# Performance work log

Hardware: AMD Instinct MI355X
Metric: run time of the kernel (lower is better)

Reference implementation:

```python
import jax, jax.numpy as jnp
import numpy as np

B, T, C, H = 2, 2048, 1024, 16
HD = C // H          # head_dim = 64
RD = HD // 2         # rotary half-dim = 32


def _rope_tables(T, rd, base=10000.0):
    inv_freq = 1.0 / (base ** (np.arange(rd, dtype=np.float32) / rd))
    t = np.arange(T, dtype=np.float32)
    ang = np.outer(t, inv_freq)  # [T, rd]
    cos = np.cos(ang)[None, :, None, :]  # [1,T,1,rd]
    sin = np.sin(ang)[None, :, None, :]
    return jnp.asarray(cos), jnp.asarray(sin)


def setup_inputs() -> dict:
    key = jax.random.key(0)
    k1, k2, k3 = jax.random.split(key, 3)
    cos, sin = _rope_tables(T, RD)
    return {
        "x": jax.random.normal(k1, (B, T, C), dtype=jnp.float32),
        "cos": cos,
        "sin": sin,
        "W_qkv": jax.random.normal(k2, (C, C), dtype=jnp.float32) / np.sqrt(C),
        "W_proj": jax.random.normal(k3, (C, C), dtype=jnp.float32) / np.sqrt(C),
        "window_left": 512,
    }


def _apply_rotary(x, cos, sin):
    # x: [B,T,H,HD]
    x1, x2 = x[..., :RD], x[..., RD:]
    y1 = x1 * cos + x2 * sin
    y2 = -x1 * sin + x2 * cos
    return jnp.concatenate([y1, y2], axis=-1)


def _rms_norm(x):
    eps = jnp.finfo(x.dtype).eps
    ms = jnp.mean(jnp.square(x), axis=-1, keepdims=True)
    return x * jax.lax.rsqrt(ms + eps)


def reference(x, cos, sin, W_qkv, W_proj, window_left):
    Bx, Tx, Cx = x.shape
    scale = HD ** -0.5
    # tied QKV projection (single matmul)
    w = jnp.einsum("btc,cd->btd", x, W_qkv).reshape(Bx, Tx, H, HD)
    w = _apply_rotary(w, cos, sin)
    w = _rms_norm(w)                      # [B,T,H,HD]
    wq = jnp.transpose(w, (0, 2, 1, 3))    # [B,H,T,HD]
    dots = jnp.einsum("bhqd,bhkd->bhqk", wq, wq) * scale  # [B,H,T,T]
    # causal + sliding-window mask: allow 0 <= (q - k) <= window_left
    i = jnp.arange(Tx)[:, None]
    j = jnp.arange(Tx)[None, :]
    dist = i - j
    allowed = (dist >= 0) & ((window_left <= 0) | (dist <= window_left))
    dots = jnp.where(allowed, dots, -jnp.inf)
    attn = jax.nn.softmax(dots, axis=-1)
    out = jnp.einsum("bhqk,bhkd->bhqd", attn, wq)
    out = jnp.transpose(out, (0, 2, 1, 3)).reshape(Bx, Tx, Cx)
    return jnp.einsum("btc,cd->btd", out, W_proj)
```

## Files before the change

kernel.cpp:

```cpp
#include <hip/hip_runtime.h>
#include <hip/hip_bf16.h>

typedef __bf16 bf16_t;
typedef __bf16 bf16x4 __attribute__((ext_vector_type(4)));
typedef __bf16 bf16x8 __attribute__((ext_vector_type(8)));
typedef float f32x4 __attribute__((ext_vector_type(4)));

#define B_ 2
#define T_ 2048
#define C_ 1024
#define H_ 16
#define HD_ 64
#define RD_ 32
#define M_ (B_ * T_)

__global__ __launch_bounds__(256) void k_prep(const float* __restrict__ x,
                                              bf16_t* __restrict__ xb,
                                              const float* __restrict__ Wq,
                                              bf16_t* __restrict__ wqt,
                                              const float* __restrict__ Wp,
                                              bf16_t* __restrict__ wpt) {
    const int bid = blockIdx.x;
    if (bid < 4096) {
        int i = bid * 256 + threadIdx.x;
        float4 v = reinterpret_cast<const float4*>(x)[i];
        bf16x4 o;
        o[0] = (bf16_t)v.x; o[1] = (bf16_t)v.y; o[2] = (bf16_t)v.z; o[3] = (bf16_t)v.w;
        reinterpret_cast<bf16x4*>(xb)[i] = o;
    } else {
        __shared__ float tile[32][33];
        int b2 = bid - 4096;
        const float* W = (b2 < 1024) ? Wq : Wp;
        bf16_t* Wt = (b2 < 1024) ? wqt : wpt;
        b2 &= 1023;
        const int n0 = (b2 & 31) * 32, k0 = (b2 >> 5) * 32;
        const int tx = threadIdx.x & 31, ty = threadIdx.x >> 5;
        for (int i = ty; i < 32; i += 8)
            tile[i][tx] = W[(size_t)(k0 + i) * C_ + n0 + tx];
        __syncthreads();
        for (int i = ty; i < 32; i += 8)
            Wt[(size_t)(n0 + i) * C_ + k0 + tx] = (bf16_t)tile[tx][i];
    }
}

template <bool FUSED>
__global__ __launch_bounds__(256) void k_gemm(const bf16_t* __restrict__ A,
                                              const bf16_t* __restrict__ Bt,
                                              float* __restrict__ C,
                                              const float* __restrict__ ct,
                                              const float* __restrict__ st,
                                              bf16_t* __restrict__ qp,
                                              bf16_t* __restrict__ vp,
                                              int M, int N, int K) {
    constexpr int SMEM_BYTES = FUSED ? 52224 : 49152;
    __shared__ __align__(16) char smem[SMEM_BYTES];
    bf16_t* As = (bf16_t*)smem;
    bf16_t* Bs = (bf16_t*)(smem + 32768);
    const int tid = threadIdx.x;
    const int lane = tid & 63, w = tid >> 6;
    const int wr = w >> 1, wc = w & 1;
    const int g = lane >> 4, li = lane & 15;
    const int bid = blockIdx.x;
    const int work = (bid & 7) * 64 + (bid >> 3);
    const int bx = work & 15;
    const int by = work >> 4;
    const size_t rowA0 = (size_t)by * 128;
    const size_t colB0 = (size_t)bx * 64;
    const bf16_t* Ab = A + rowA0 * K;
    const bf16_t* Bb = Bt + colB0 * K;
    f32x4 acc[4][2] = {};

    const int lr = lane >> 3;
    const int swc = ((lane & 7) ^ lr) * 8;

    auto stage = [&](int buf, int k0) {
        bf16_t* Ad = As + buf * 8192 + (w * 8) * 64;
        bf16_t* Bd = Bs + buf * 4096 + (w * 8) * 64;
#pragma unroll
        for (int a = 0; a < 4; ++a) {
            const bf16_t* src = Ab + (size_t)(a * 32 + w * 8 + lr) * K + k0 + swc;
            __builtin_amdgcn_global_load_lds(
                (const __attribute__((address_space(1))) void*)src,
                (__attribute__((address_space(3))) void*)(Ad + a * 32 * 64), 16, 0, 0);
        }
#pragma unroll
        for (int bq = 0; bq < 2; ++bq) {
            const bf16_t* src = Bb + (size_t)(bq * 32 + w * 8 + lr) * K + k0 + swc;
            __builtin_amdgcn_global_load_lds(
                (const __attribute__((address_space(1))) void*)src,
                (__attribute__((address_space(3))) void*)(Bd + bq * 32 * 64), 16, 0, 0);
        }
    };

    stage(0, 0);
    __syncthreads();
    int cur = 0;
    const int NT = K >> 6;
    for (int kt = 0; kt < NT; ++kt) {
        if (kt < NT - 1) stage(cur ^ 1, (kt + 1) << 6);
        bf16x8 af[4][2], bfr[2][2];
#pragma unroll
        for (int i = 0; i < 4; ++i) {
            const int row = wr * 64 + i * 16 + li;
#pragma unroll
            for (int kk = 0; kk < 2; ++kk)
                af[i][kk] = *(const bf16x8*)(As + cur * 8192 + row * 64 +
                                             (((kk * 4 + g) ^ (li & 7)) * 8));
        }
#pragma unroll
        for (int j = 0; j < 2; ++j) {
            const int row = wc * 32 + j * 16 + li;
#pragma unroll
            for (int kk = 0; kk < 2; ++kk)
                bfr[j][kk] = *(const bf16x8*)(Bs + cur * 4096 + row * 64 +
                                              (((kk * 4 + g) ^ (li & 7)) * 8));
        }
#pragma unroll
        for (int i = 0; i < 4; ++i)
#pragma unroll
            for (int j = 0; j < 2; ++j)
#pragma unroll
                for (int kk = 0; kk < 2; ++kk)
                    acc[i][j] = __builtin_amdgcn_mfma_f32_16x16x32_bf16(
                        af[i][kk], bfr[j][kk], acc[i][j], 0, 0, 0);
        __syncthreads();
        cur ^= 1;
    }

    if constexpr (!FUSED) {
#pragma unroll
        for (int i = 0; i < 4; ++i)
#pragma unroll
            for (int j = 0; j < 2; ++j)
#pragma unroll
                for (int r = 0; r < 4; ++r) {
                    size_t row = rowA0 + wr * 64 + i * 16 + g * 4 + r;
                    size_t col = colB0 + wc * 32 + j * 16 + li;
                    C[row * N + col] = acc[i][j][r];
                }
    } else {
        float* ot = (float*)smem;
        bf16_t* qs = (bf16_t*)(smem + 34816);
#pragma unroll
        for (int i = 0; i < 4; ++i)
#pragma unroll
            for (int j = 0; j < 2; ++j)
#pragma unroll
                for (int r = 0; r < 4; ++r)
                    ot[(wr * 64 + i * 16 + g * 4 + r) * 68 + wc * 32 + j * 16 + li] =
                        acc[i][j][r];
        __syncthreads();
        const int bb = (int)(rowA0 >> 11);
        {
            const int row = tid >> 1, half = tid & 1;
            const int t = ((int)rowA0 + row) & 2047;
            const float* own = ot + row * 68 + half * 32;
            const float* par = ot + row * 68 + (half ^ 1) * 32;
            const float* cp = ct + (size_t)t * RD_;
            const float* sp = st + (size_t)t * RD_;
            float y[32];
            float sq = 0.f;
#pragma unroll
            for (int c4 = 0; c4 < 8; ++c4) {
                float4 xo = ((const float4*)own)[c4];
                float4 xp = ((const float4*)par)[c4];
                float4 cc = ((const float4*)cp)[c4];
                float4 ss = ((const float4*)sp)[c4];
                float* yy = y + c4 * 4;
                if (half == 0) {
                    yy[0] = xo.x * cc.x + xp.x * ss.x;
                    yy[1] = xo.y * cc.y + xp.y * ss.y;
                    yy[2] = xo.z * cc.z + xp.z * ss.z;
                    yy[3] = xo.w * cc.w + xp.w * ss.w;
                } else {
                    yy[0] = xo.x * cc.x - xp.x * ss.x;
                    yy[1] = xo.y * cc.y - xp.y * ss.y;
                    yy[2] = xo.z * cc.z - xp.z * ss.z;
                    yy[3] = xo.w * cc.w - xp.w * ss.w;
                }
                sq += yy[0] * yy[0] + yy[1] * yy[1] + yy[2] * yy[2] + yy[3] * yy[3];
            }
            sq += __shfl_xor(sq, 1);
            const float rn = rsqrtf(sq * (1.0f / 64.0f) + 1.1920929e-7f);
            bf16_t yb[32];
#pragma unroll
            for (int e = 0; e < 32; ++e) yb[e] = (bf16_t)(y[e] * rn);
            bf16_t* qpb = qp + ((size_t)(bb * H_ + bx) * 128 + (t >> 4)) * 1024;
#pragma unroll
            for (int c8 = 0; c8 < 4; ++c8) {
                const int chunk = (half * 4 + c8) * 16 + (t & 15);
                *(bf16x8*)(qpb + chunk * 8) = *(const bf16x8*)(yb + c8 * 8);
            }
#pragma unroll
            for (int e = 0; e < 32; ++e)
                qs[(half * 32 + e) * 136 + row] = yb[e];
        }
        __syncthreads();
        {
            const int d = tid >> 2, jc4 = tid & 3;
            const int tt0 = (int)((rowA0 & 2047) >> 6);
            bf16_t* vpb = vp + ((size_t)(bb * H_ + bx) * 32) * 4096;
#pragma unroll
            for (int c = 0; c < 4; ++c) {
                const int jc = jc4 * 4 + c;
                bf16x8 v8 = *(const bf16x8*)(qs + d * 136 + jc * 8);
                bf16_t* dst = vpb + (size_t)(tt0 + (jc >> 3)) * 4096 +
                              ((d >> 4) * 8 + (jc & 7)) * 128 + (d & 15) * 8;
                *(bf16x8*)dst = v8;
            }
        }
    }
}

__global__ __launch_bounds__(256, 4) void k_attn(const bf16_t* __restrict__ qp,
                                                 const bf16_t* __restrict__ vp,
                                                 bf16_t* __restrict__ aout,
                                                 const int* __restrict__ wlp) {
    __shared__ bf16_t pb[4][16][40];
    const int tid = threadIdx.x;
    const int lane = tid & 63, w = tid >> 6;
    const int g = lane >> 4, li = lane & 15;
    const int bid = blockIdx.x;
    const int work = (bid & 7) * 128 + (bid >> 3);
    const int tb = work & 31;
    const int h = (work >> 5) & 15;
    const int b = work >> 9;
    const int Q0 = tb * 64;
    const bf16_t* bq = qp + (size_t)(b * H_ + h) * 131072;
    const bf16_t* bv = vp + (size_t)(b * H_ + h) * 131072;
    const int wl = wlp[0];
    const int wle = (wl <= 0 || wl > T_) ? T_ : wl;
    const int qw = Q0 + w * 16;
    const int qg = qw + li;

    const int fo = (g * 16 + li) * 8;
    const int vo = g * 128 + li * 8;

    bf16x8 aq[2];
    aq[0] = *(const bf16x8*)(bq + (size_t)(qw >> 4) * 1024 + fo);
    aq[1] = *(const bf16x8*)(bq + (size_t)(qw >> 4) * 1024 + fo + 512);

    f32x4 o[4] = {};
    float m = -1e30f, l = 0.f;
    const float SC = 0.125f * 1.44269504089f;

    const int kb0 = (qw > wle) ? ((qw - wle) >> 6) : 0;
    const int kb1 = qw >> 6;

    for (int kb = kb0; kb <= kb1; ++kb) {
        const int J0 = kb << 6;
        const bf16_t* kt = bq + (size_t)kb * 4096;
        const bf16_t* vt = bv + (size_t)kb * 4096;
        bf16x8 kf[2][4];
#pragma unroll
        for (int ks = 0; ks < 2; ++ks)
#pragma unroll
            for (int nb = 0; nb < 4; ++nb)
                kf[ks][nb] = *(const bf16x8*)(kt + nb * 1024 + ks * 512 + fo);
        f32x4 s4[4] = {};
        __builtin_amdgcn_s_setprio(1);
#pragma unroll
        for (int ks = 0; ks < 2; ++ks)
#pragma unroll
            for (int nb = 0; nb < 4; ++nb)
                s4[nb] = __builtin_amdgcn_mfma_f32_16x16x32_bf16(kf[ks][nb], aq[ks],
                                                                 s4[nb], 0, 0, 0);
        __builtin_amdgcn_s_setprio(0);
        bf16x8 vf[2][4];
#pragma unroll
        for (int ks = 0; ks < 2; ++ks)
#pragma unroll
            for (int dnb = 0; dnb < 4; ++dnb)
                vf[ks][dnb] = *(const bf16x8*)(vt + dnb * 1024 + ks * 512 + vo);
        float sv[4][4];
        float mn = m;
#pragma unroll
        for (int nb = 0; nb < 4; ++nb)
#pragma unroll
            for (int r = 0; r < 4; ++r) {
                const int j = J0 + nb * 16 + g * 4 + r;
                const int dist = qg - j;
                float x = s4[nb][r] * SC;
                sv[nb][r] = (dist >= 0 && dist <= wle) ? x : -__builtin_inff();
                mn = fmaxf(mn, sv[nb][r]);
            }
        mn = fmaxf(mn, __shfl_xor(mn, 16));
        mn = fmaxf(mn, __shfl_xor(mn, 32));
        const float al = exp2f(m - mn);
        m = mn;
        float la = 0.f;
#pragma unroll
        for (int nb = 0; nb < 4; ++nb)
#pragma unroll
            for (int r = 0; r < 4; ++r) {
                float pv = exp2f(sv[nb][r] - m);
                sv[nb][r] = pv;
                la += pv;
            }
        la += __shfl_xor(la, 16);
        la += __shfl_xor(la, 32);
        l = l * al + la;
        float alq[4];
#pragma unroll
        for (int r = 0; r < 4; ++r) alq[r] = __shfl(al, g * 4 + r);
#pragma unroll
        for (int dnb = 0; dnb < 4; ++dnb)
#pragma unroll
            for (int r = 0; r < 4; ++r) o[dnb][r] *= alq[r];
#pragma unroll
        for (int ks = 0; ks < 2; ++ks) {
#pragma unroll
            for (int nb2 = 0; nb2 < 2; ++nb2) {
                const int nb = ks * 2 + nb2;
                bf16x4 pk;
                pk[0] = (bf16_t)sv[nb][0]; pk[1] = (bf16_t)sv[nb][1];
                pk[2] = (bf16_t)sv[nb][2]; pk[3] = (bf16_t)sv[nb][3];
                *reinterpret_cast<bf16x4*>(&pb[w][li][nb2 * 16 + g * 4]) = pk;
            }
            bf16x8 pa = *reinterpret_cast<const bf16x8*>(&pb[w][li][g * 8]);
            __builtin_amdgcn_s_setprio(1);
#pragma unroll
            for (int dnb = 0; dnb < 4; ++dnb)
                o[dnb] = __builtin_amdgcn_mfma_f32_16x16x32_bf16(pa, vf[ks][dnb],
                                                                 o[dnb], 0, 0, 0);
            __builtin_amdgcn_s_setprio(0);
        }
    }

    const float rli = 1.0f / l;
    float rlq[4];
#pragma unroll
    for (int r = 0; r < 4; ++r) rlq[r] = __shfl(rli, g * 4 + r);
#pragma unroll
    for (int dnb = 0; dnb < 4; ++dnb)
#pragma unroll
        for (int r = 0; r < 4; ++r) {
            size_t t = (size_t)qw + g * 4 + r;
            aout[((size_t)b * T_ + t) * C_ + h * 64 + dnb * 16 + li] =
                (bf16_t)(o[dnb][r] * rlq[r]);
        }
}

extern "C" void kernel_launch(void* const* d_in, const int* in_sizes, int n_in,
                              void* d_out, int out_size, void* d_ws, size_t ws_size,
                              hipStream_t stream) {
    const float* x     = (const float*)d_in[0];
    const float* ct    = (const float*)d_in[1];
    const float* st    = (const float*)d_in[2];
    const float* Wqkv  = (const float*)d_in[3];
    const float* Wproj = (const float*)d_in[4];
    const int*   wl    = (const int*)d_in[5];
    float* out = (float*)d_out;
    char* ws = (char*)d_ws;

    bf16_t* xb    = (bf16_t*)(ws);
    bf16_t* wqkvt = (bf16_t*)(ws + (8ull << 20));
    bf16_t* wprot = (bf16_t*)(ws + (10ull << 20));
    bf16_t* qp    = (bf16_t*)(ws + (12ull << 20));
    bf16_t* vp    = (bf16_t*)(ws + (20ull << 20));
    bf16_t* ao    = (bf16_t*)(ws + (28ull << 20));

    k_prep<<<dim3(6144), dim3(256), 0, stream>>>(x, xb, Wqkv, wqkvt, Wproj, wprot);
    k_gemm<true><<<dim3(512), dim3(256), 0, stream>>>(xb, wqkvt, nullptr, ct, st,
                                                      qp, vp, M_, C_, C_);
    k_attn<<<dim3(1024), dim3(256), 0, stream>>>(qp, vp, ao, wl);
    k_gemm<false><<<dim3(512), dim3(256), 0, stream>>>(ao, wprot, out, nullptr, nullptr,
                                                       nullptr, nullptr, M_, C_, C_);
}
```

Before: 69.14 us.

## Double-buffer K fragments, skip masking on interior tiles, lazily rescale softmax

The attention inner loop now prefetches the next key block's fragments into a ping-pong register buffer while the current block's scores are computed. Tiles that lie wholly inside the causal sliding window skip the per-element mask. The online softmax only updates the running max and rescales the accumulator when some row's max grows by more than 8 in log2 space. These aim to hide global-load latency and cut VALU and shuffle work, at the cost of higher register pressure from the extra K buffer.

```diff
diff --git a/kernel.cpp b/kernel.cpp
--- a/kernel.cpp
+++ b/kernel.cpp
@@ -247,85 +247,106 @@
     const int kb0 = (qw > wle) ? ((qw - wle) >> 6) : 0;
     const int kb1 = qw >> 6;
 
-    for (int kb = kb0; kb <= kb1; ++kb) {
-        const int J0 = kb << 6;
-        const bf16_t* kt = bq + (size_t)kb * 4096;
-        const bf16_t* vt = bv + (size_t)kb * 4096;
-        bf16x8 kf[2][4];
-#pragma unroll
-        for (int ks = 0; ks < 2; ++ks)
-#pragma unroll
-            for (int nb = 0; nb < 4; ++nb)
-                kf[ks][nb] = *(const bf16x8*)(kt + nb * 1024 + ks * 512 + fo);
-        f32x4 s4[4] = {};
-        __builtin_amdgcn_s_setprio(1);
-#pragma unroll
-        for (int ks = 0; ks < 2; ++ks)
-#pragma unroll
-            for (int nb = 0; nb < 4; ++nb)
-                s4[nb] = __builtin_amdgcn_mfma_f32_16x16x32_bf16(kf[ks][nb], aq[ks],
-                                                                 s4[nb], 0, 0, 0);
-        __builtin_amdgcn_s_setprio(0);
-        bf16x8 vf[2][4];
-#pragma unroll
-        for (int ks = 0; ks < 2; ++ks)
-#pragma unroll
-            for (int dnb = 0; dnb < 4; ++dnb)
-                vf[ks][dnb] = *(const bf16x8*)(vt + dnb * 1024 + ks * 512 + vo);
-        float sv[4][4];
-        float mn = m;
+    bf16x8 kfA[2][4], kfB[2][4], vf[2][4];
+#pragma unroll
+    for (int ks = 0; ks < 2; ++ks)
 #pragma unroll
         for (int nb = 0; nb < 4; ++nb)
-#pragma unroll
-            for (int r = 0; r < 4; ++r) {
-                const int j = J0 + nb * 16 + g * 4 + r;
-                const int dist = qg - j;
-                float x = s4[nb][r] * SC;
-                sv[nb][r] = (dist >= 0 && dist <= wle) ? x : -__builtin_inff();
-                mn = fmaxf(mn, sv[nb][r]);
-            }
-        mn = fmaxf(mn, __shfl_xor(mn, 16));
-        mn = fmaxf(mn, __shfl_xor(mn, 32));
-        const float al = exp2f(m - mn);
-        m = mn;
-        float la = 0.f;
-#pragma unroll
-        for (int nb = 0; nb < 4; ++nb)
-#pragma unroll
-            for (int r = 0; r < 4; ++r) {
-                float pv = exp2f(sv[nb][r] - m);
-                sv[nb][r] = pv;
-                la += pv;
-            }
-        la += __shfl_xor(la, 16);
-        la += __shfl_xor(la, 32);
-        l = l * al + la;
-        float alq[4];
-#pragma unroll
-        for (int r = 0; r < 4; ++r) alq[r] = __shfl(al, g * 4 + r);
-#pragma unroll
-        for (int dnb = 0; dnb < 4; ++dnb)
-#pragma unroll
-            for (int r = 0; r < 4; ++r) o[dnb][r] *= alq[r];
-#pragma unroll
-        for (int ks = 0; ks < 2; ++ks) {
-#pragma unroll
-            for (int nb2 = 0; nb2 < 2; ++nb2) {
-                const int nb = ks * 2 + nb2;
-                bf16x4 pk;
-                pk[0] = (bf16_t)sv[nb][0]; pk[1] = (bf16_t)sv[nb][1];
-                pk[2] = (bf16_t)sv[nb][2]; pk[3] = (bf16_t)sv[nb][3];
-                *reinterpret_cast<bf16x4*>(&pb[w][li][nb2 * 16 + g * 4]) = pk;
-            }
-            bf16x8 pa = *reinterpret_cast<const bf16x8*>(&pb[w][li][g * 8]);
-            __builtin_amdgcn_s_setprio(1);
-#pragma unroll
-            for (int dnb = 0; dnb < 4; ++dnb)
-                o[dnb] = __builtin_amdgcn_mfma_f32_16x16x32_bf16(pa, vf[ks][dnb],
-                                                                 o[dnb], 0, 0, 0);
-            __builtin_amdgcn_s_setprio(0);
-        }
-    }
+            kfA[ks][nb] = *(const bf16x8*)(bq + (size_t)kb0 * 4096 + nb * 1024 +
+                                           ks * 512 + fo);
+    int kb = kb0;
+
+#define ATTN_STEP(KC, KN)                                                              \
+    {                                                                                  \
+        const int J0 = kb << 6;                                                        \
+        f32x4 s4[4] = {};                                                              \
+        __builtin_amdgcn_s_setprio(1);                                                 \
+        _Pragma("unroll") for (int ks = 0; ks < 2; ++ks)                               \
+        _Pragma("unroll") for (int nb = 0; nb < 4; ++nb)                               \
+            s4[nb] = __builtin_amdgcn_mfma_f32_16x16x32_bf16(KC[ks][nb], aq[ks],       \
+                                                             s4[nb], 0, 0, 0);         \
+        __builtin_amdgcn_s_setprio(0);                                                 \
+        if (kb < kb1) {                                                                \
+            const bf16_t* kt = bq + (size_t)(kb + 1) * 4096;                           \
+            _Pragma("unroll") for (int ks = 0; ks < 2; ++ks)                           \
+            _Pragma("unroll") for (int nb = 0; nb < 4; ++nb)                           \
+                KN[ks][nb] = *(const bf16x8*)(kt + nb * 1024 + ks * 512 + fo);         \
+        }                                                                              \
+        {                                                                              \
+            const bf16_t* vt = bv + (size_t)kb * 4096;                                 \
+            _Pragma("unroll") for (int ks = 0; ks < 2; ++ks)                           \
+            _Pragma("unroll") for (int dnb = 0; dnb < 4; ++dnb)                        \
+                vf[ks][dnb] = *(const bf16x8*)(vt + dnb * 1024 + ks * 512 + vo);       \
+        }                                                                              \
+        const bool interior = (J0 + 63 <= qw) && (J0 >= qw + 15 - wle);                \
+        float tm = -__builtin_inff();                                                  \
+        if (interior) {                                                                \
+            _Pragma("unroll") for (int nb = 0; nb < 4; ++nb)                           \
+            _Pragma("unroll") for (int r = 0; r < 4; ++r) {                            \
+                s4[nb][r] *= SC;                                                       \
+                tm = fmaxf(tm, s4[nb][r]);                                             \
+            }                                                                          \
+        } else {                                                                       \
+            _Pragma("unroll") for (int nb = 0; nb < 4; ++nb)                           \
+            _Pragma("unroll") for (int r = 0; r < 4; ++r) {                            \
+                const int j = J0 + nb * 16 + g * 4 + r;                                \
+                const int dist = qg - j;                                               \
+                float x = s4[nb][r] * SC;                                              \
+                s4[nb][r] = (dist >= 0 && dist <= wle) ? x : -__builtin_inff();        \
+                tm = fmaxf(tm, s4[nb][r]);                                             \
+            }                                                                          \
+        }                                                                              \
+        tm = fmaxf(tm, __shfl_xor(tm, 16));                                            \
+        tm = fmaxf(tm, __shfl_xor(tm, 32));                                            \
+        const bool skip = __all(tm <= m + 8.0f);                                       \
+        float al = 1.0f;                                                               \
+        if (!skip) {                                                                   \
+            al = exp2f(m - tm);                                                        \
+            m = tm;                                                                    \
+        }                                                                              \
+        float la = 0.f;                                                                \
+        _Pragma("unroll") for (int nb = 0; nb < 4; ++nb)                               \
+        _Pragma("unroll") for (int r = 0; r < 4; ++r) {                                \
+            float pv = exp2f(s4[nb][r] - m);                                           \
+            s4[nb][r] = pv;                                                            \
+            la += pv;                                                                  \
+        }                                                                              \
+        la += __shfl_xor(la, 16);                                                      \
+        la += __shfl_xor(la, 32);                                                      \
+        if (!skip) {                                                                   \
+            l = l * al + la;                                                           \
+            float alq[4];                                                              \
+            _Pragma("unroll") for (int r = 0; r < 4; ++r)                              \
+                alq[r] = __shfl(al, g * 4 + r);                                        \
+            _Pragma("unroll") for (int dnb = 0; dnb < 4; ++dnb)                        \
+            _Pragma("unroll") for (int r = 0; r < 4; ++r) o[dnb][r] *= alq[r];         \
+        } else {                                                                       \
+            l += la;                                                                   \
+        }                                                                              \
+        _Pragma("unroll") for (int ks = 0; ks < 2; ++ks) {                             \
+            _Pragma("unroll") for (int nb2 = 0; nb2 < 2; ++nb2) {                      \
+                const int nb = ks * 2 + nb2;                                           \
+                bf16x4 pk;                                                             \
+                pk[0] = (bf16_t)s4[nb][0]; pk[1] = (bf16_t)s4[nb][1];                  \
+                pk[2] = (bf16_t)s4[nb][2]; pk[3] = (bf16_t)s4[nb][3];                  \
+                *reinterpret_cast<bf16x4*>(&pb[w][li][nb2 * 16 + g * 4]) = pk;         \
+            }                                                                          \
+            bf16x8 pa = *reinterpret_cast<const bf16x8*>(&pb[w][li][g * 8]);           \
+            __builtin_amdgcn_s_setprio(1);                                             \
+            _Pragma("unroll") for (int dnb = 0; dnb < 4; ++dnb)                        \
+                o[dnb] = __builtin_amdgcn_mfma_f32_16x16x32_bf16(pa, vf[ks][dnb],      \
+                                                                 o[dnb], 0, 0, 0);     \
+            __builtin_amdgcn_s_setprio(0);                                             \
+        }                                                                              \
+    }
+
+    while (true) {
+        ATTN_STEP(kfA, kfB)
+        if (++kb > kb1) break;
+        ATTN_STEP(kfB, kfA)
+        if (++kb > kb1) break;
+    }
+#undef ATTN_STEP
 
     const float rli = 1.0f / l;
     float rlq[4];
```

Result: slower. 131.0 us (+89.5%).
